# Kernel tuning notes

Hardware: AMD Instinct MI355X
Metric: run time of the kernel (lower is better)

Reference implementation:

```python
import jax, jax.numpy as jnp
import numpy as np

# (mul_l0, mul_l1, mul_l2) multiplicities per stage, mirroring the torch Model
FEATS = [(7, 0, 0), (6, 3, 1), (6, 3, 1), (14, 6, 3), (14, 6, 3),
         (30, 12, 6), (30, 12, 6), (32, 16, 8), (512, 0, 0)]
STRIDES = [2, 1, 2, 1, 2, 1, 2, 1]
KSIZE, PAD = 5, 4
BATCH, GRID, N_OUT = 16, 64, 20

def _dims(f):
    return f[0] + 3 * f[1] + 5 * f[2]

def _gates(f):
    return f[1] + f[2]


def setup_inputs() -> dict:
    key = jax.random.key(0)
    ks = jax.random.split(key, 11)
    inp = {"x": jax.random.normal(ks[0], (BATCH, _dims(FEATS[0]), GRID, GRID, GRID), jnp.float32)}
    for i in range(8):
        cin = _dims(FEATS[i])
        cout = _dims(FEATS[i + 1]) + _gates(FEATS[i + 1])
        std = 1.0 / np.sqrt(cin * KSIZE ** 3)
        inp[f"W{i+1}"] = (jax.random.normal(ks[i + 1], (cout, cin, KSIZE, KSIZE, KSIZE), jnp.float32) * std)
    inp["linW"] = jax.random.normal(ks[9], (N_OUT, 512), jnp.float32) * (1.0 / np.sqrt(512))
    inp["linb"] = jnp.zeros((N_OUT,), jnp.float32)
    return inp


def gated_block(x, W, f_out, stride):
    # conv3d, size 5, padding 4, given stride
    y = jax.lax.conv_general_dilated(
        x, W, window_strides=(stride,) * 3, padding=[(PAD, PAD)] * 3,
        dimension_numbers=("NCDHW", "OIDHW", "NCDHW"))
    # batch norm over batch + spatial dims (no affine)
    m = y.mean((0, 2, 3, 4), keepdims=True)
    v = y.var((0, 2, 3, 4), keepdims=True)
    y = (y - m) * jax.lax.rsqrt(v + 1e-5)
    m0, m1, m2 = f_out
    d = m0 + 3 * m1 + 5 * m2
    parts = [jax.nn.relu(y[:, :m0])]  # scalar (l=0) channels: relu
    if m1 + m2 > 0:
        g = jax.nn.sigmoid(y[:, d:])  # one gate scalar per non-scalar irrep
        B = y.shape[0]
        sp = y.shape[2:]
        if m1 > 0:  # l=1 irreps (3 components each), gated
            v1 = y[:, m0:m0 + 3 * m1].reshape(B, m1, 3, *sp) * g[:, :m1, None]
            parts.append(v1.reshape(B, 3 * m1, *sp))
        if m2 > 0:  # l=2 irreps (5 components each), gated
            v2 = y[:, m0 + 3 * m1:d].reshape(B, m2, 5, *sp) * g[:, m1:m1 + m2, None]
            parts.append(v2.reshape(B, 5 * m2, *sp))
    return jnp.concatenate(parts, axis=1) if len(parts) > 1 else parts[0]


def reference(x, W1, W2, W3, W4, W5, W6, W7, W8, linW, linb):
    Ws = [W1, W2, W3, W4, W5, W6, W7, W8]
    h = x
    for i in range(8):
        h = gated_block(h, Ws[i], FEATS[i + 1], STRIDES[i])
    # AvgSpacial: mean over all spatial positions -> [B, 512]
    pooled = h.reshape(h.shape[0], h.shape[1], -1).mean(-1)
    return pooled @ linW.T + linb
```

## Files before the change

kernel.cpp:

```cpp
#include <hip/hip_runtime.h>
#include <hip/hip_bf16.h>

typedef __bf16 bf16x8 __attribute__((ext_vector_type(8)));
typedef float f32x4 __attribute__((ext_vector_type(4)));
typedef unsigned int uint4v __attribute__((ext_vector_type(4)));
typedef unsigned short ushortT;
typedef ushortT ushort8v __attribute__((ext_vector_type(8)));

__device__ __forceinline__ ushortT f2b(float f) {
    __bf16 b = (__bf16)f;
    return __builtin_bit_cast(ushortT, b);
}

__device__ __forceinline__ unsigned xcd_swz(unsigned bx, unsigned nwg) {
    unsigned q = nwg >> 3, r = nwg & 7, xcd = bx & 7, off = bx >> 3;
    return (xcd < r ? xcd * (q + 1) : r * (q + 1) + (xcd - r) * q) + off;
}

__global__ __launch_bounds__(256) void pack_x(const float* __restrict__ x,
                                              ushortT* __restrict__ xb)
{
    long e = (long)blockIdx.x * 256 + threadIdx.x;
    if (e >= 5971968L) return;
    int wp_ = (int)(e % 72); long r = e / 72;
    int hp = (int)(r % 72); r /= 72;
    int dp = (int)(r % 72); int b = (int)(r / 72);
    ushort8v v = (ushort8v)0;
    int dd = dp - 4, hh = hp - 4, ww = wp_ - 4;
    if ((unsigned)dd < 64u && (unsigned)hh < 64u && (unsigned)ww < 64u) {
        int sp = (dd * 64 + hh) * 64 + ww;
        #pragma unroll
        for (int c = 0; c < 7; ++c)
            v[c] = f2b(x[((size_t)(b * 7 + c)) * 262144 + sp]);
    }
    *(ushort8v*)(xb + e * 8) = v;
}

__global__ void pack_w(const float* __restrict__ W, ushortT* __restrict__ wp,
                       int Cin, int CINP, int Cout, int NW, int KSTEPS, int total)
{
    int e = blockIdx.x * 256 + threadIdx.x;
    if (e >= total) return;
    int j = e & 7;
    int r = e >> 3;
    int c = r % NW; r /= NW;
    int q = r & 3; r >>= 2;
    int s = r % KSTEPS;
    int nby = r / KSTEPS;
    int k = s * 32 + q * 8 + j;
    int tap = k / CINP;
    int ci = k - tap * CINP;
    int n = nby * NW + c;
    float v = 0.f;
    if (tap < 125 && ci < Cin && n < Cout)
        v = W[((size_t)n * Cin + ci) * 125 + tap];
    wp[e] = f2b(v);
}

__global__ void pack_w_lds2(const float* __restrict__ W, ushortT* __restrict__ wp,
                            int Cin, int Cout, int NW, int CHUNKS, int total)
{
    int e = blockIdx.x * 256 + threadIdx.x;
    if (e >= total) return;
    int j = e & 7;
    int r = e >> 3;
    int n = r % NW; r /= NW;
    int q = r & 3; r >>= 2;
    int s = r % 32; r /= 32;
    int c = r % CHUNKS;
    int nby = r / CHUNKS;
    int tap = 4 * s + q;
    int ci = c * 8 + j;
    int nn = nby * NW + n;
    float v = 0.f;
    if (tap < 125 && ci < Cin && nn < Cout)
        v = W[((size_t)nn * Cin + ci) * 125 + tap];
    wp[e] = f2b(v);
}

template<int CINP, int INDP, int OUTD, int STRIDE, int COUT, int NFRAG, int KSTEPS, int KTOT>
__global__ __launch_bounds__(256)
void conv_ig(const ushortT* __restrict__ xcl, const ushortT* __restrict__ wp,
             float* __restrict__ y)
{
    constexpr int S3 = OUTD * OUTD * OUTD;
    constexpr long MTOT = 16L * S3;
    constexpr int NW = NFRAG * 16;
    const int t = threadIdx.x, lane = t & 63, wave = t >> 6;
    const unsigned bx = xcd_swz(blockIdx.x, gridDim.x);
    const long mbase = (long)bx * 256 + wave * 64;
    const int slot = lane >> 4;

    unsigned rb[4];
    #pragma unroll
    for (int i = 0; i < 4; ++i) {
        long m = mbase + i * 16 + (lane & 15);
        if (m >= MTOT) m = MTOT - 1;
        int b = (int)(m / S3); int sp = (int)(m % S3);
        int od = sp / (OUTD * OUTD); int oh = (sp / OUTD) % OUTD; int ow = sp % OUTD;
        rb[i] = (unsigned)(((((b * INDP) + od * STRIDE) * INDP + oh * STRIDE) * INDP
                            + ow * STRIDE) * CINP);
    }
    const ushortT* wptr = wp + ((size_t)((blockIdx.y * KSTEPS) * 4 + slot) * NW
                                + (lane & 15)) * 8;

    f32x4 acc[NFRAG][4];
    #pragma unroll
    for (int n = 0; n < NFRAG; ++n)
        #pragma unroll
        for (int i = 0; i < 4; ++i) acc[n][i] = (f32x4)0.f;

    for (int s = 0; s < KSTEPS; ++s) {
        const int k0 = s * 32 + slot * 8;
        const int tap = k0 / CINP;
        const int ci = k0 - tap * CINP;
        const int kd = tap / 25;
        const int rr = tap - kd * 25;
        const int kh = rr / 5;
        const int kw = rr - kh * 5;
        const unsigned toff = (unsigned)(((kd * INDP + kh) * INDP + kw) * CINP + ci);
        const bool valid = k0 < KTOT;
        uint4v a[4];
        #pragma unroll
        for (int i = 0; i < 4; ++i) {
            unsigned idx = valid ? (rb[i] + toff) : 0u;
            a[i] = *(const uint4v*)(xcl + idx);
        }
        uint4v bv[NFRAG];
        #pragma unroll
        for (int n = 0; n < NFRAG; ++n)
            bv[n] = *(const uint4v*)(wptr + (size_t)s * (4 * NW * 8) + n * 128);
        #pragma unroll
        for (int n = 0; n < NFRAG; ++n) {
            bf16x8 bb = __builtin_bit_cast(bf16x8, bv[n]);
            #pragma unroll
            for (int i = 0; i < 4; ++i)
                acc[n][i] = __builtin_amdgcn_mfma_f32_16x16x32_bf16(
                    __builtin_bit_cast(bf16x8, a[i]), bb, acc[n][i], 0, 0, 0);
        }
    }

    const int rbase = (lane >> 4) * 4;
    #pragma unroll
    for (int n = 0; n < NFRAG; ++n) {
        int nn = blockIdx.y * NW + n * 16 + (lane & 15);
        if (nn >= COUT) continue;
        #pragma unroll
        for (int i = 0; i < 4; ++i) {
            #pragma unroll
            for (int r = 0; r < 4; ++r) {
                long mm = mbase + i * 16 + rbase + r;
                if (mm < MTOT) y[(size_t)mm * COUT + nn] = acc[n][i][r];
            }
        }
    }
}

template<int CHUNKS, int INDP, int OUTD, int TD, int TH, int COUT, int NFRAG, int MFRAG>
__global__ __launch_bounds__(256)
void conv_lds2(const ushortT* __restrict__ xcl, const ushortT* __restrict__ wp,
               float* __restrict__ y)
{
    constexpr int CH = CHUNKS * 8;
    constexpr int PD = TD + 4, PH = TH + 4, PW = INDP;
    constexpr int P3 = PD * PH * PW;
    constexpr int ROWS = TD * TH * OUTD;
    constexpr int NW = NFRAG * 16;
    constexpr int NTD = (OUTD + TD - 1) / TD;
    constexpr int NTH = (OUTD + TH - 1) / TH;
    constexpr size_t PERNBY = (size_t)CHUNKS * 32 * 4 * NW * 8;
    static_assert(ROWS <= MFRAG * 64, "row coverage");

    __shared__ __align__(16) ushortT patch[P3 * 8];
    __shared__ int tofftab[128];

    const int t = threadIdx.x, lane = t & 63, wave = t >> 6;
    const unsigned bt = xcd_swz(blockIdx.x, gridDim.x);
    const int img = bt / (NTD * NTH);
    const int t2 = bt % (NTD * NTH);
    const int od0 = (t2 / NTH) * TD;
    const int oh0 = (t2 % NTH) * TH;

    if (t < 128) {
        int tap = t < 125 ? t : 0;
        int kd = tap / 25, rr = tap - kd * 25, kh = rr / 5, kw = rr - kh * 5;
        tofftab[t] = (t < 125) ? ((kd * PH + kh) * PW + kw) : 0;
    }

    const int r16 = lane & 15, q = lane >> 4;

    int rb[MFRAG];
    #pragma unroll
    for (int i = 0; i < MFRAG; ++i) {
        int r = wave * (MFRAG * 16) + i * 16 + r16;
        if (r >= ROWS) r = ROWS - 1;
        int td = r / (TH * OUTD); int rem = r - td * (TH * OUTD);
        int th = rem / OUTD; int ow = rem - th * OUTD;
        rb[i] = (td * PH + th) * PW + ow;
    }

    const ushortT* wb = wp + (size_t)blockIdx.y * PERNBY + ((size_t)q * NW + r16) * 8;
    const ushortT* src0 = xcl + (size_t)img * INDP * INDP * INDP * CH;

    f32x4 acc[NFRAG][MFRAG];
    #pragma unroll
    for (int n = 0; n < NFRAG; ++n)
        #pragma unroll
        for (int i = 0; i < MFRAG; ++i) acc[n][i] = (f32x4)0.f;

    for (int c = 0; c < CHUNKS; ++c) {
        __syncthreads();
        for (int u = t; u < P3; u += 256) {
            int pd = u / (PH * PW); int pr = u - pd * (PH * PW);
            int ph = pr / PW; int pw = pr - ph * PW;
            int gd = od0 + pd; if (gd > INDP - 1) gd = INDP - 1;
            int gh = oh0 + ph; if (gh > INDP - 1) gh = INDP - 1;
            const ushortT* sp_ = src0 + (((size_t)gd * INDP + gh) * INDP + pw) * CH
                                 + c * 8;
            uint4v v = *(const uint4v*)sp_;
            *(uint4v*)&patch[u * 8] = v;
        }
        __syncthreads();
        const ushortT* wc = wb + (size_t)c * (32 * 4 * NW * 8);
        for (int s = 0; s < 32; ++s) {
            int toffv = tofftab[4 * s + q];
            uint4v bv[NFRAG];
            #pragma unroll
            for (int n = 0; n < NFRAG; ++n)
                bv[n] = *(const uint4v*)(wc + (size_t)s * (4 * NW * 8) + n * 128);
            #pragma unroll
            for (int i = 0; i < MFRAG; ++i) {
                bf16x8 av = *(const bf16x8*)&patch[(rb[i] + toffv) * 8];
                #pragma unroll
                for (int n = 0; n < NFRAG; ++n)
                    acc[n][i] = __builtin_amdgcn_mfma_f32_16x16x32_bf16(
                        av, __builtin_bit_cast(bf16x8, bv[n]), acc[n][i], 0, 0, 0);
            }
        }
    }

    #pragma unroll
    for (int i = 0; i < MFRAG; ++i) {
        #pragma unroll
        for (int vr = 0; vr < 4; ++vr) {
            int r = wave * (MFRAG * 16) + i * 16 + q * 4 + vr;
            if (r >= ROWS) continue;
            int td = r / (TH * OUTD); int rem = r - td * (TH * OUTD);
            int th = rem / OUTD; int ow = rem - th * OUTD;
            int od = od0 + td, oh = oh0 + th;
            if (od >= OUTD || oh >= OUTD) continue;
            size_t row = ((size_t)img * OUTD + od) * (size_t)(OUTD * OUTD)
                       + (size_t)oh * OUTD + ow;
            #pragma unroll
            for (int n = 0; n < NFRAG; ++n) {
                int nn = blockIdx.y * NW + n * 16 + r16;
                if (nn < COUT) y[row * COUT + nn] = acc[n][i][vr];
            }
        }
    }
}

__global__ __launch_bounds__(256)
void bn_partial_cl(const float* __restrict__ y, float* __restrict__ part,
                   long rows, int C, int crlog2)
{
    const int t = threadIdx.x;
    const int CR = 1 << crlog2;
    const int c = t & (CR - 1);
    const int r0 = t >> crlog2;
    const int rstep = 256 >> crlog2;
    float s0 = 0.f, q0 = 0.f;
    const bool has = c < C;
    for (long r = (long)blockIdx.x * rstep + r0; r < rows; r += 256L * rstep) {
        if (has) { float v = y[(size_t)r * C + c]; s0 += v; q0 = fmaf(v, v, q0); }
    }
    __shared__ float l0[256], l1[256];
    l0[t] = s0; l1[t] = q0; __syncthreads();
    if (t < CR) {
        for (int j = 1; j < rstep; ++j) { s0 += l0[t + j * CR]; q0 += l1[t + j * CR]; }
        if (t < C) {
            part[((size_t)blockIdx.x * 256 + t) * 2]     = s0;
            part[((size_t)blockIdx.x * 256 + t) * 2 + 1] = q0;
        }
    }
}

__global__ void bn_finalize(const float* __restrict__ part, float* __restrict__ stats,
                            int C, float invN)
{
    int c = threadIdx.x;
    if (c >= C) return;
    float s = 0.f, q = 0.f;
    for (int k = 0; k < 256; ++k) {
        s += part[((size_t)k * 256 + c) * 2];
        q += part[((size_t)k * 256 + c) * 2 + 1];
    }
    float mean = s * invN;
    float var = q * invN - mean * mean;
    stats[2 * c] = mean;
    stats[2 * c + 1] = rsqrtf(var + 1e-5f);
}

template<int CINP, int INDP, int OUTD>
__global__ __launch_bounds__(256)
void act_pad(const float* __restrict__ y, const float* __restrict__ stats,
             ushortT* __restrict__ h, int COUT, int d, int m0, int m1)
{
    constexpr long TOT = 16L * INDP * INDP * INDP * CINP;
    long e = (long)blockIdx.x * 256 + threadIdx.x;
    if (e >= TOT) return;
    int c = (int)(e % CINP); long r = e / CINP;
    int wp_ = (int)(r % INDP); r /= INDP;
    int hp = (int)(r % INDP); r /= INDP;
    int dp = (int)(r % INDP); int b = (int)(r / INDP);
    float o = 0.f;
    int dd = dp - 4, hh = hp - 4, ww = wp_ - 4;
    if (c < d && (unsigned)dd < (unsigned)OUTD && (unsigned)hh < (unsigned)OUTD
        && (unsigned)ww < (unsigned)OUTD) {
        long row = ((b * (long)OUTD + dd) * OUTD + hh) * OUTD + ww;
        float v = (y[row * COUT + c] - stats[2 * c]) * stats[2 * c + 1];
        if (c < m0) {
            o = fmaxf(v, 0.f);
        } else {
            int gi = (c < m0 + 3 * m1) ? (d + (c - m0) / 3)
                                       : (d + m1 + (c - m0 - 3 * m1) / 5);
            float g = (y[row * COUT + gi] - stats[2 * gi]) * stats[2 * gi + 1];
            o = v / (1.f + __expf(-g));
        }
    }
    h[e] = f2b(o);
}

__global__ __launch_bounds__(256)
void pool_partial(const float* __restrict__ y, const float* __restrict__ stats,
                  float* __restrict__ pp)
{
    const int b = blockIdx.x, slab = blockIdx.y, c = threadIdx.x;
    const float mu = stats[2 * c], iv = stats[2 * c + 1];
    float a = 0.f;
    for (int i = 0; i < 64; ++i)
        a += fmaxf((y[((size_t)b * 4096 + slab * 64 + i) * 256 + c] - mu) * iv, 0.f);
    pp[(size_t)(b * 64 + slab) * 256 + c] = a;
}

__global__ void pool_final(const float* __restrict__ pp, float* __restrict__ pooled)
{
    const int b = blockIdx.x, c = threadIdx.x;
    float a = 0.f;
    for (int s = 0; s < 64; ++s) a += pp[(size_t)(b * 64 + s) * 256 + c];
    pooled[b * 512 + c] = a * (1.f / 4096.f);
}

__global__ void linear20(const float* __restrict__ pooled, const float* __restrict__ lw,
                         const float* __restrict__ lb, float* __restrict__ out)
{
    const int n = blockIdx.x, b = blockIdx.y;
    const float* p = pooled + b * 512;
    const float* w = lw + n * 512;
    float s = 0.f;
    for (int c = threadIdx.x; c < 512; c += 64) s = fmaf(p[c], w[c], s);
    for (int o = 32; o > 0; o >>= 1) s += __shfl_down(s, o);
    if (threadIdx.x == 0) out[b * 20 + n] = s + lb[n];
}

extern "C" void kernel_launch(void* const* d_in, const int* in_sizes, int n_in,
                              void* d_out, int out_size, void* d_ws, size_t ws_size,
                              hipStream_t stream) {
    const float* x = (const float*)d_in[0];
    const float* Wf[8];
    for (int i = 0; i < 8; ++i) Wf[i] = (const float*)d_in[1 + i];
    const float* linW = (const float*)d_in[9];
    const float* linb = (const float*)d_in[10];
    float* out = (float*)d_out;
    float* ws = (float*)d_ws;

    const size_t OFF_Y    = 0;
    const size_t OFF_H    = 21070848;
    const size_t OFF_WP   = 44958720;
    const size_t OFF_PART = 51628800;
    const size_t OFF_PP   = 51759872;
    const size_t OFF_ST   = 52022016;
    const size_t OFF_PL   = 52023040;
    const size_t NEEDF    = 52031232;
    if (ws_size < NEEDF * sizeof(float)) return;

    float* yb = ws + OFF_Y;
    ushortT* H = (ushortT*)(ws + OFF_H);
    ushortT* wpb = (ushortT*)(ws + OFF_WP);
    float* part = ws + OFF_PART;
    float* pp = ws + OFF_PP;
    float* stats = ws + OFF_ST;
    float* pooled = ws + OFF_PL;

    const size_t WPO_S1 = 0;
    const size_t WPO_S3 = 32768;
    const size_t WPO_S5 = 225280;
    const size_t WPO_S7 = 995328;
    const size_t WPO_S2 = 2723328;
    const size_t WPO_S4 = 2854400;
    const size_t WPO_S6 = 3378688;
    const size_t WPO_S8 = 4951552;

    pack_x<<<23328, 256, 0, stream>>>(x, H);
    pack_w<<<(32768 + 255) / 256, 256, 0, stream>>>(Wf[0], wpb + WPO_S1, 7, 8, 24, 32, 32, 32768);
    pack_w<<<(192512 + 255) / 256, 256, 0, stream>>>(Wf[2], wpb + WPO_S3, 20, 24, 56, 64, 94, 192512);
    pack_w<<<(770048 + 255) / 256, 256, 0, stream>>>(Wf[4], wpb + WPO_S5, 47, 48, 114, 64, 188, 770048);
    pack_w<<<(1728000 + 255) / 256, 256, 0, stream>>>(Wf[6], wpb + WPO_S7, 96, 96, 144, 48, 375, 1728000);
    pack_w_lds2<<<(131072 + 255) / 256, 256, 0, stream>>>(Wf[1], wpb + WPO_S2, 20, 24, 32, 4, 131072);
    pack_w_lds2<<<(524288 + 255) / 256, 256, 0, stream>>>(Wf[3], wpb + WPO_S4, 47, 56, 64, 8, 524288);
    pack_w_lds2<<<(1572864 + 255) / 256, 256, 0, stream>>>(Wf[5], wpb + WPO_S6, 96, 114, 64, 12, 1572864);
    pack_w_lds2<<<(8388608 + 255) / 256, 256, 0, stream>>>(Wf[7], wpb + WPO_S8, 120, 512, 64, 16, 8388608);

    long rows;

    rows = 628864;
    conv_ig<8, 72, 34, 2, 24, 2, 32, 1000><<<dim3(2457, 1), 256, 0, stream>>>(H, wpb + WPO_S1, yb);
    bn_partial_cl<<<256, 256, 0, stream>>>(yb, part, rows, 24, 5);
    bn_finalize<<<1, 256, 0, stream>>>(part, stats, 24, 1.f / (float)rows);
    act_pad<32, 42, 34><<<148176, 256, 0, stream>>>(yb, stats, H, 24, 20, 6, 3);

    rows = 877952;
    conv_lds2<4, 42, 38, 2, 3, 24, 2, 4><<<dim3(3952, 1), 256, 0, stream>>>(H, wpb + WPO_S2, yb);
    bn_partial_cl<<<256, 256, 0, stream>>>(yb, part, rows, 24, 5);
    bn_finalize<<<1, 256, 0, stream>>>(part, stats, 24, 1.f / (float)rows);
    act_pad<24, 46, 38><<<146004, 256, 0, stream>>>(yb, stats, H, 24, 20, 6, 3);

    rows = 148176;
    conv_ig<24, 46, 21, 2, 56, 4, 94, 3000><<<dim3(579, 1), 256, 0, stream>>>(H, wpb + WPO_S3, yb);
    bn_partial_cl<<<256, 256, 0, stream>>>(yb, part, rows, 56, 6);
    bn_finalize<<<1, 256, 0, stream>>>(part, stats, 56, 1.f / (float)rows);
    act_pad<64, 29, 21><<<97556, 256, 0, stream>>>(yb, stats, H, 56, 47, 14, 6);

    rows = 250000;
    conv_lds2<8, 29, 25, 2, 5, 56, 4, 4><<<dim3(1040, 1), 256, 0, stream>>>(H, wpb + WPO_S4, yb);
    bn_partial_cl<<<256, 256, 0, stream>>>(yb, part, rows, 56, 6);
    bn_finalize<<<1, 256, 0, stream>>>(part, stats, 56, 1.f / (float)rows);
    act_pad<48, 33, 25><<<107811, 256, 0, stream>>>(yb, stats, H, 56, 47, 14, 6);

    rows = 54000;
    conv_ig<48, 33, 15, 2, 114, 4, 188, 6000><<<dim3(211, 2), 256, 0, stream>>>(H, wpb + WPO_S5, yb);
    bn_partial_cl<<<256, 256, 0, stream>>>(yb, part, rows, 114, 7);
    bn_finalize<<<1, 256, 0, stream>>>(part, stats, 114, 1.f / (float)rows);
    act_pad<96, 23, 15><<<73002, 256, 0, stream>>>(yb, stats, H, 114, 96, 30, 12);

    rows = 109744;
    conv_lds2<12, 23, 19, 2, 6, 114, 4, 4><<<dim3(640, 2), 256, 0, stream>>>(H, wpb + WPO_S6, yb);
    bn_partial_cl<<<256, 256, 0, stream>>>(yb, part, rows, 114, 7);
    bn_finalize<<<1, 256, 0, stream>>>(part, stats, 114, 1.f / (float)rows);
    act_pad<96, 27, 19><<<118098, 256, 0, stream>>>(yb, stats, H, 114, 96, 30, 12);

    rows = 27648;
    conv_ig<96, 27, 12, 2, 144, 3, 375, 12000><<<dim3(108, 3), 256, 0, stream>>>(H, wpb + WPO_S7, yb);
    bn_partial_cl<<<256, 256, 0, stream>>>(yb, part, rows, 144, 8);
    bn_finalize<<<1, 256, 0, stream>>>(part, stats, 144, 1.f / (float)rows);
    act_pad<128, 20, 12><<<64000, 256, 0, stream>>>(yb, stats, H, 144, 120, 32, 16);

    rows = 65536;
    for (int h8 = 0; h8 < 2; ++h8) {
        conv_lds2<16, 20, 16, 4, 4, 256, 4, 4><<<dim3(256, 4), 256, 0, stream>>>(
            H, wpb + WPO_S8 + (size_t)h8 * 4194304, yb);
        bn_partial_cl<<<256, 256, 0, stream>>>(yb, part, rows, 256, 8);
        bn_finalize<<<1, 256, 0, stream>>>(part, stats, 256, 1.f / (float)rows);
        pool_partial<<<dim3(16, 64), 256, 0, stream>>>(yb, stats, pp);
        pool_final<<<16, 256, 0, stream>>>(pp, pooled + h8 * 256);
    }
    linear20<<<dim3(20, 16), 64, 0, stream>>>(pooled, linW, linb, out);
}
```

Baseline: 3.777 ms.

## Trim padded input channels and merge final-stage halves into one 512-channel pass

```diff
diff --git a/kernel.cpp b/kernel.cpp
--- a/kernel.cpp
+++ b/kernel.cpp
@@ -294,6 +294,37 @@
     for (int k = 0; k < 256; ++k) {
         s += part[((size_t)k * 256 + c) * 2];
         q += part[((size_t)k * 256 + c) * 2 + 1];
+    }
+    float mean = s * invN;
+    float var = q * invN - mean * mean;
+    stats[2 * c] = mean;
+    stats[2 * c + 1] = rsqrtf(var + 1e-5f);
+}
+
+__global__ __launch_bounds__(256)
+void bn_partial512(const float* __restrict__ y, float* __restrict__ part, long rows)
+{
+    const int t = threadIdx.x;
+    float s0 = 0.f, q0 = 0.f, s1 = 0.f, q1 = 0.f;
+    for (long r = blockIdx.x; r < rows; r += 256) {
+        const float* row = y + (size_t)r * 512;
+        float v0 = row[t];       s0 += v0; q0 = fmaf(v0, v0, q0);
+        float v1 = row[t + 256]; s1 += v1; q1 = fmaf(v1, v1, q1);
+    }
+    part[((size_t)blockIdx.x * 512 + t) * 2]           = s0;
+    part[((size_t)blockIdx.x * 512 + t) * 2 + 1]       = q0;
+    part[((size_t)blockIdx.x * 512 + t + 256) * 2]     = s1;
+    part[((size_t)blockIdx.x * 512 + t + 256) * 2 + 1] = q1;
+}
+
+__global__ void bn_finalize512(const float* __restrict__ part, float* __restrict__ stats,
+                               float invN)
+{
+    int c = blockIdx.x * 256 + threadIdx.x;
+    float s = 0.f, q = 0.f;
+    for (int k = 0; k < 256; ++k) {
+        s += part[((size_t)k * 512 + c) * 2];
+        q += part[((size_t)k * 512 + c) * 2 + 1];
     }
     float mean = s * invN;
     float var = q * invN - mean * mean;
@@ -332,23 +363,33 @@
 }
 
 __global__ __launch_bounds__(256)
-void pool_partial(const float* __restrict__ y, const float* __restrict__ stats,
-                  float* __restrict__ pp)
-{
-    const int b = blockIdx.x, slab = blockIdx.y, c = threadIdx.x;
-    const float mu = stats[2 * c], iv = stats[2 * c + 1];
-    float a = 0.f;
-    for (int i = 0; i < 64; ++i)
-        a += fmaxf((y[((size_t)b * 4096 + slab * 64 + i) * 256 + c] - mu) * iv, 0.f);
-    pp[(size_t)(b * 64 + slab) * 256 + c] = a;
-}
-
-__global__ void pool_final(const float* __restrict__ pp, float* __restrict__ pooled)
-{
-    const int b = blockIdx.x, c = threadIdx.x;
-    float a = 0.f;
-    for (int s = 0; s < 64; ++s) a += pp[(size_t)(b * 64 + s) * 256 + c];
-    pooled[b * 512 + c] = a * (1.f / 4096.f);
+void pool_partial512(const float* __restrict__ y, const float* __restrict__ stats,
+                     float* __restrict__ pp)
+{
+    const int b = blockIdx.x, slab = blockIdx.y, t = threadIdx.x;
+    const int c0 = t, c1 = t + 256;
+    const float mu0 = stats[2 * c0], iv0 = stats[2 * c0 + 1];
+    const float mu1 = stats[2 * c1], iv1 = stats[2 * c1 + 1];
+    float a0 = 0.f, a1 = 0.f;
+    for (int i = 0; i < 64; ++i) {
+        const float* row = y + ((size_t)b * 4096 + slab * 64 + i) * 512;
+        a0 += fmaxf((row[c0] - mu0) * iv0, 0.f);
+        a1 += fmaxf((row[c1] - mu1) * iv1, 0.f);
+    }
+    pp[(size_t)(b * 64 + slab) * 512 + c0] = a0;
+    pp[(size_t)(b * 64 + slab) * 512 + c1] = a1;
+}
+
+__global__ void pool_final512(const float* __restrict__ pp, float* __restrict__ pooled)
+{
+    const int b = blockIdx.x, t = threadIdx.x;
+    float a0 = 0.f, a1 = 0.f;
+    for (int s = 0; s < 64; ++s) {
+        a0 += pp[(size_t)(b * 64 + s) * 512 + t];
+        a1 += pp[(size_t)(b * 64 + s) * 512 + t + 256];
+    }
+    pooled[b * 512 + t]       = a0 * (1.f / 4096.f);
+    pooled[b * 512 + t + 256] = a1 * (1.f / 4096.f);
 }
 
 __global__ void linear20(const float* __restrict__ pooled, const float* __restrict__ lw,
@@ -375,13 +416,13 @@
     float* ws = (float*)d_ws;
 
     const size_t OFF_Y    = 0;
-    const size_t OFF_H    = 21070848;
-    const size_t OFF_WP   = 44958720;
-    const size_t OFF_PART = 51628800;
-    const size_t OFF_PP   = 51759872;
-    const size_t OFF_ST   = 52022016;
-    const size_t OFF_PL   = 52023040;
-    const size_t NEEDF    = 52031232;
+    const size_t OFF_H    = 33554432;
+    const size_t OFF_WP   = 57442304;
+    const size_t OFF_PART = 63768320;
+    const size_t OFF_PP   = 64030464;
+    const size_t OFF_ST   = 64554752;
+    const size_t OFF_PL   = 64555776;
+    const size_t NEEDF    = 64563968;
     if (ws_size < NEEDF * sizeof(float)) return;
 
     float* yb = ws + OFF_Y;
@@ -397,19 +438,19 @@
     const size_t WPO_S5 = 225280;
     const size_t WPO_S7 = 995328;
     const size_t WPO_S2 = 2723328;
-    const size_t WPO_S4 = 2854400;
-    const size_t WPO_S6 = 3378688;
-    const size_t WPO_S8 = 4951552;
+    const size_t WPO_S4 = 2821632;
+    const size_t WPO_S6 = 3214848;
+    const size_t WPO_S8 = 4787712;
 
     pack_x<<<23328, 256, 0, stream>>>(x, H);
     pack_w<<<(32768 + 255) / 256, 256, 0, stream>>>(Wf[0], wpb + WPO_S1, 7, 8, 24, 32, 32, 32768);
     pack_w<<<(192512 + 255) / 256, 256, 0, stream>>>(Wf[2], wpb + WPO_S3, 20, 24, 56, 64, 94, 192512);
     pack_w<<<(770048 + 255) / 256, 256, 0, stream>>>(Wf[4], wpb + WPO_S5, 47, 48, 114, 64, 188, 770048);
     pack_w<<<(1728000 + 255) / 256, 256, 0, stream>>>(Wf[6], wpb + WPO_S7, 96, 96, 144, 48, 375, 1728000);
-    pack_w_lds2<<<(131072 + 255) / 256, 256, 0, stream>>>(Wf[1], wpb + WPO_S2, 20, 24, 32, 4, 131072);
-    pack_w_lds2<<<(524288 + 255) / 256, 256, 0, stream>>>(Wf[3], wpb + WPO_S4, 47, 56, 64, 8, 524288);
+    pack_w_lds2<<<(98304 + 255) / 256, 256, 0, stream>>>(Wf[1], wpb + WPO_S2, 20, 24, 32, 3, 98304);
+    pack_w_lds2<<<(393216 + 255) / 256, 256, 0, stream>>>(Wf[3], wpb + WPO_S4, 47, 56, 64, 6, 393216);
     pack_w_lds2<<<(1572864 + 255) / 256, 256, 0, stream>>>(Wf[5], wpb + WPO_S6, 96, 114, 64, 12, 1572864);
-    pack_w_lds2<<<(8388608 + 255) / 256, 256, 0, stream>>>(Wf[7], wpb + WPO_S8, 120, 512, 64, 16, 8388608);
+    pack_w_lds2<<<(7864320 + 255) / 256, 256, 0, stream>>>(Wf[7], wpb + WPO_S8, 120, 512, 64, 15, 7864320);
 
     long rows;
 
@@ -417,10 +458,10 @@
     conv_ig<8, 72, 34, 2, 24, 2, 32, 1000><<<dim3(2457, 1), 256, 0, stream>>>(H, wpb + WPO_S1, yb);
     bn_partial_cl<<<256, 256, 0, stream>>>(yb, part, rows, 24, 5);
     bn_finalize<<<1, 256, 0, stream>>>(part, stats, 24, 1.f / (float)rows);
-    act_pad<32, 42, 34><<<148176, 256, 0, stream>>>(yb, stats, H, 24, 20, 6, 3);
+    act_pad<24, 42, 34><<<111132, 256, 0, stream>>>(yb, stats, H, 24, 20, 6, 3);
 
     rows = 877952;
-    conv_lds2<4, 42, 38, 2, 3, 24, 2, 4><<<dim3(3952, 1), 256, 0, stream>>>(H, wpb + WPO_S2, yb);
+    conv_lds2<3, 42, 38, 2, 3, 24, 2, 4><<<dim3(3952, 1), 256, 0, stream>>>(H, wpb + WPO_S2, yb);
     bn_partial_cl<<<256, 256, 0, stream>>>(yb, part, rows, 24, 5);
     bn_finalize<<<1, 256, 0, stream>>>(part, stats, 24, 1.f / (float)rows);
     act_pad<24, 46, 38><<<146004, 256, 0, stream>>>(yb, stats, H, 24, 20, 6, 3);
@@ -429,10 +470,10 @@
     conv_ig<24, 46, 21, 2, 56, 4, 94, 3000><<<dim3(579, 1), 256, 0, stream>>>(H, wpb + WPO_S3, yb);
     bn_partial_cl<<<256, 256, 0, stream>>>(yb, part, rows, 56, 6);
     bn_finalize<<<1, 256, 0, stream>>>(part, stats, 56, 1.f / (float)rows);
-    act_pad<64, 29, 21><<<97556, 256, 0, stream>>>(yb, stats, H, 56, 47, 14, 6);
+    act_pad<48, 29, 21><<<73167, 256, 0, stream>>>(yb, stats, H, 56, 47, 14, 6);
 
     rows = 250000;
-    conv_lds2<8, 29, 25, 2, 5, 56, 4, 4><<<dim3(1040, 1), 256, 0, stream>>>(H, wpb + WPO_S4, yb);
+    conv_lds2<6, 29, 25, 2, 5, 56, 4, 4><<<dim3(1040, 1), 256, 0, stream>>>(H, wpb + WPO_S4, yb);
     bn_partial_cl<<<256, 256, 0, stream>>>(yb, part, rows, 56, 6);
     bn_finalize<<<1, 256, 0, stream>>>(part, stats, 56, 1.f / (float)rows);
     act_pad<48, 33, 25><<<107811, 256, 0, stream>>>(yb, stats, H, 56, 47, 14, 6);
@@ -453,16 +494,14 @@
     conv_ig<96, 27, 12, 2, 144, 3, 375, 12000><<<dim3(108, 3), 256, 0, stream>>>(H, wpb + WPO_S7, yb);
     bn_partial_cl<<<256, 256, 0, stream>>>(yb, part, rows, 144, 8);
     bn_finalize<<<1, 256, 0, stream>>>(part, stats, 144, 1.f / (float)rows);
-    act_pad<128, 20, 12><<<64000, 256, 0, stream>>>(yb, stats, H, 144, 120, 32, 16);
+    act_pad<120, 20, 12><<<60000, 256, 0, stream>>>(yb, stats, H, 144, 120, 32, 16);
 
     rows = 65536;
-    for (int h8 = 0; h8 < 2; ++h8) {
-        conv_lds2<16, 20, 16, 4, 4, 256, 4, 4><<<dim3(256, 4), 256, 0, stream>>>(
-            H, wpb + WPO_S8 + (size_t)h8 * 4194304, yb);
-        bn_partial_cl<<<256, 256, 0, stream>>>(yb, part, rows, 256, 8);
-        bn_finalize<<<1, 256, 0, stream>>>(part, stats, 256, 1.f / (float)rows);
-        pool_partial<<<dim3(16, 64), 256, 0, stream>>>(yb, stats, pp);
-        pool_final<<<16, 256, 0, stream>>>(pp, pooled + h8 * 256);
-    }
+    conv_lds2<15, 20, 16, 4, 4, 512, 4, 4><<<dim3(256, 8), 256, 0, stream>>>(
+        H, wpb + WPO_S8, yb);
+    bn_partial512<<<256, 256, 0, stream>>>(yb, part, rows);
+    bn_finalize512<<<2, 256, 0, stream>>>(part, stats, 1.f / (float)rows);
+    pool_partial512<<<dim3(16, 64), 256, 0, stream>>>(yb, stats, pp);
+    pool_final512<<<16, 256, 0, stream>>>(pp, pooled);
     linear20<<<dim3(20, 16), 64, 0, stream>>>(pooled, linW, linb, out);
 }
```

Result: faster. 3.531 ms (median of 3 runs) (-6.5%).
